# Kernel optimization log

Hardware: AMD Instinct MI355X
Metric: run time of the kernel (lower is better)

## Reference

```python
import jax, jax.numpy as jnp
import numpy as np

B, M, N, C, L = 4, 500, 500, 91, 3


def _lsa(cost):
    """Exact linear sum assignment (shortest augmenting path / LAPJV),
    numpy port of scipy's rectangular_lsap for a square cost matrix.
    Returns col4row: col4row[i] = column assigned to row i."""
    n = cost.shape[0]
    u = np.zeros(n, dtype=np.float64)
    v = np.zeros(n, dtype=np.float64)
    col4row = np.full(n, -1, dtype=np.int64)
    row4col = np.full(n, -1, dtype=np.int64)
    cost = cost.astype(np.float64)
    for cur_row in range(n):
        min_val = 0.0
        i = cur_row
        remaining = np.ones(n, dtype=bool)
        shortest = np.full(n, np.inf)
        path = np.full(n, -1, dtype=np.int64)
        SR = []
        sink = -1
        while sink == -1:
            SR.append(i)
            r = min_val + cost[i] - u[i] - v
            better = remaining & (r < shortest)
            shortest = np.where(better, r, shortest)
            path = np.where(better, i, path)
            masked = np.where(remaining, shortest, np.inf)
            j = int(np.argmin(masked))
            min_val = masked[j]
            remaining[j] = False
            if row4col[j] == -1:
                sink = j
            else:
                i = int(row4col[j])
        u[cur_row] += min_val
        sr = np.array(SR[1:], dtype=np.int64)
        if sr.size:
            u[sr] += min_val - shortest[col4row[sr]]
        scanned_cols = ~remaining
        v[scanned_cols] -= min_val - shortest[scanned_cols]
        # augment along the alternating path
        j = sink
        while True:
            i = int(path[j])
            row4col[j] = i
            col4row[i], j = j, col4row[i]
            if i == cur_row:
                break
    return col4row


def _assignment(cost_np):
    """(B, M, N) numpy cost -> (B, M) row->col mapping (square => all assigned)."""
    return np.stack([_lsa(c) for c in cost_np]).astype(np.int64)


def _cost_matrix(p2_boxes, p2_logits, p1_boxes, p1_logits):
    # center L2 distance: cdist(boxes2[..., :2], boxes1[..., :2], p=2) -> (B, M, N)
    diff = p2_boxes[:, :, None, :2] - p1_boxes[:, None, :, :2]
    center_d = jnp.sqrt(jnp.sum(diff * diff, axis=-1))
    # class disparity: cdist(sigmoid(l2), sigmoid(l1), p=inf) -> (B, M, N)
    s2 = jax.nn.sigmoid(p2_logits)
    s1 = jax.nn.sigmoid(p1_logits)
    class_d = jnp.max(jnp.abs(s2[:, :, None, :] - s1[:, None, :, :]), axis=-1)
    return 0.5 * center_d + 0.5 * class_d


def _extrapolate(p2_boxes, p2_logits, p1_boxes, p1_logits, mapping, factor):
    has = mapping != -1                      # (B, M)
    m = jnp.where(has, mapping, 0)
    idx4 = jnp.broadcast_to(m[:, :, None], m.shape + (4,))
    corr_b1 = jnp.take_along_axis(p1_boxes, idx4, axis=1)
    corr_b1 = jnp.where(has[:, :, None], corr_b1, p2_boxes)
    # 'linear' dim extrapolation, clamped at 0
    pos = p2_boxes[..., 0:2] + (p2_boxes[..., 0:2] - corr_b1[..., 0:2]) * factor
    dim = jnp.maximum(p2_boxes[..., 2:4] + (p2_boxes[..., 2:4] - corr_b1[..., 2:4]) * factor, 0.0)
    boxes3 = jnp.concatenate([pos, dim], axis=2)
    nclass = p1_logits.shape[-1]
    idxc = jnp.broadcast_to(m[:, :, None], m.shape + (nclass,))
    corr_l1 = jnp.take_along_axis(p1_logits, idxc, axis=1)
    corr_l1 = jnp.where(has[:, :, None], corr_l1, 0.0)
    logits3 = 0.5 * (p2_logits + corr_l1)
    return boxes3, logits3


def setup_inputs() -> dict:
    key = jax.random.key(0)
    k1, k2, k3, k4, k5 = jax.random.split(key, 5)
    pred1_boxes = jax.random.uniform(k1, (B, N, 4), dtype=jnp.float32)
    pred1_logits = jax.random.normal(k2, (B, N, C), dtype=jnp.float32)
    pred2_boxes = jax.random.uniform(k3, (B, M, 4), dtype=jnp.float32)
    pred2_logits = jax.random.normal(k4, (B, M, C), dtype=jnp.float32)
    # strictly increasing timestamps so offsets are positive
    temporal_offsets = jnp.cumsum(
        jax.random.uniform(k5, (B, L), minval=0.1, maxval=1.0, dtype=jnp.float32), axis=1)
    return {
        "pred1_boxes": pred1_boxes,
        "pred1_logits": pred1_logits,
        "pred2_boxes": pred2_boxes,
        "pred2_logits": pred2_logits,
        "temporal_offsets": temporal_offsets,
    }


def reference(pred1_boxes, pred1_logits, pred2_boxes, pred2_logits, temporal_offsets):
    cost = _cost_matrix(pred2_boxes, pred2_logits, pred1_boxes, pred1_logits)
    mapping = jnp.asarray(_assignment(np.asarray(cost)))  # (B, M) int64
    first = temporal_offsets[:, 1] - temporal_offsets[:, 0]
    second = temporal_offsets[:, 2] - temporal_offsets[:, 1]
    factor = (second / first)[:, None, None]
    boxes3, logits3 = _extrapolate(pred2_boxes, pred2_logits,
                                   pred1_boxes, pred1_logits, mapping, factor)
    return boxes3, logits3
```

## Files before the change

### kernel.cpp

```cpp
#include <hip/hip_runtime.h>
#include <math.h>

#define Bq 4
#define Mq 500
#define Nq 500
#define Cq 91
#define NPHASE 5

__device__ __forceinline__ float sigmoidf_(float x) {
    return 1.0f / (1.0f + expf(-x));
}

__global__ __launch_bounds__(256) void cost_kernel(
    const float* __restrict__ p1_boxes, const float* __restrict__ p1_logits,
    const float* __restrict__ p2_boxes, const float* __restrict__ p2_logits,
    float* __restrict__ cost)
{
    __shared__ float s2t[16][Cq + 1];
    __shared__ float s1t[16][Cq + 1];
    __shared__ float b2x[16], b2y[16], b1x[16], b1y[16];
    const int b  = blockIdx.z;
    const int i0 = blockIdx.y * 16;
    const int j0 = blockIdx.x * 16;
    const int tid = threadIdx.x;

    for (int t = tid; t < 16 * Cq; t += 256) {
        const int r = t / Cq, c = t - r * Cq;
        const int i = min(i0 + r, Mq - 1);
        const int j = min(j0 + r, Nq - 1);
        s2t[r][c] = sigmoidf_(p2_logits[((size_t)b * Mq + i) * Cq + c]);
        s1t[r][c] = sigmoidf_(p1_logits[((size_t)b * Nq + j) * Cq + c]);
    }
    if (tid < 16) {
        const int i = min(i0 + tid, Mq - 1);
        const int j = min(j0 + tid, Nq - 1);
        b2x[tid] = p2_boxes[((size_t)b * Mq + i) * 4 + 0];
        b2y[tid] = p2_boxes[((size_t)b * Mq + i) * 4 + 1];
        b1x[tid] = p1_boxes[((size_t)b * Nq + j) * 4 + 0];
        b1y[tid] = p1_boxes[((size_t)b * Nq + j) * 4 + 1];
    }
    __syncthreads();

    const int ty = tid >> 4, tx = tid & 15;
    const int i = i0 + ty, j = j0 + tx;
    if (i < Mq && j < Nq) {
        float mx = 0.0f;
        #pragma unroll 7
        for (int c = 0; c < Cq; ++c)
            mx = fmaxf(mx, fabsf(s2t[ty][c] - s1t[tx][c]));
        const float dx = b2x[ty] - b1x[tx];
        const float dy = b2y[ty] - b1y[tx];
        const float cd = sqrtf(dx * dx + dy * dy);
        cost[((size_t)b * Mq + i) * Nq + j] = 0.5f * cd + 0.5f * mx;
    }
}

__global__ __launch_bounds__(256) void colred_kernel(
    const float* __restrict__ cost, float* __restrict__ v0, int* __restrict__ amin)
{
    const int j = blockIdx.x * 256 + threadIdx.x;
    const int b = blockIdx.y;
    if (j >= Nq) return;
    const float* __restrict__ cb = cost + (size_t)b * Mq * Nq;
    float best = INFINITY;
    int bi = 0;
    #pragma unroll 4
    for (int i = 0; i < Mq; ++i) {
        const float c = cb[(size_t)i * Nq + j];
        if (c < best) { best = c; bi = i; }
    }
    v0[b * Nq + j] = best;
    amin[b * Nq + j] = bi;
}

template<int CTRL>
__device__ __forceinline__ float dppminv_(float x) {
    const int moved = __builtin_amdgcn_update_dpp(
        0x7F800000, __float_as_int(x), CTRL, 0xF, 0xF, false);
    return fminf(x, __int_as_float(moved));
}
__device__ __forceinline__ float wave_min_f32_(float x) {
    x = dppminv_<0x111>(x);
    x = dppminv_<0x112>(x);
    x = dppminv_<0x114>(x);
    x = dppminv_<0x118>(x);
    x = dppminv_<0x142>(x);
    x = dppminv_<0x143>(x);
    return __int_as_float(__builtin_amdgcn_readlane(__float_as_int(x), 63));
}

__device__ __forceinline__ void pairmin_(float& va, unsigned& pa, float vb, unsigned pb) {
    const bool le = (va <= vb);
    va = fminf(va, vb);
    pa = le ? pa : pb;
}

__device__ __forceinline__ unsigned long long pack_bid_(float p, int row) {
    return ((unsigned long long)__float_as_uint(p) << 32) | (unsigned)(row + 1);
}

__global__ __launch_bounds__(1024) void auction_kernel(
    const float* __restrict__ cost, const float* __restrict__ v0,
    const int* __restrict__ amin,
    float* __restrict__ v_out, int* __restrict__ owner_out)
{
    constexpr int n = Nq;
    __shared__ float p_lds[512];
    __shared__ int   owner_lds[512];
    __shared__ int   match_lds[512];
    __shared__ unsigned long long bid_lds[512];
    __shared__ int   flist[512];
    __shared__ int   jlist[512];
    __shared__ int   nfree_lds, njl_lds;

    const float eps_tab[NPHASE] = {4e-3f, 8e-4f, 1.6e-4f, 3.2e-5f, 0.0f};
    const int   cap_tab[NPHASE] = {48, 32, 32, 32, 64};

    const int tid = threadIdx.x;
    const int lane = tid & 63;
    const int wv = tid >> 6;
    const int b = blockIdx.x;
    const float* __restrict__ cb = cost + (size_t)b * n * n;

    const unsigned init_mask = (lane < 61) ? 0xFFu : 0x0Fu;
    const int off2 = (lane < 61) ? 256 + 4 * lane : 0;

    float v0_r[8];
    {
        const float4 a0 = *(const float4*)(v0 + b * n + 4 * lane);
        const float4 a1 = *(const float4*)(v0 + b * n + off2);
        const float vv[8] = {a0.x, a0.y, a0.z, a0.w, a1.x, a1.y, a1.z, a1.w};
        #pragma unroll
        for (int k = 0; k < 8; ++k)
            v0_r[k] = ((init_mask >> k) & 1) ? vv[k] : 0.0f;
    }
    if (tid < 512) {
        p_lds[tid] = 0.0f; owner_lds[tid] = -1; match_lds[tid] = -1;
        bid_lds[tid] = 0ull;
    }
    __syncthreads();
    if (tid < n) {
        const int i0 = amin[b * n + tid];
        if (atomicCAS(&match_lds[i0], -1, tid) == -1) owner_lds[tid] = i0;
    }
    __syncthreads();

    for (int ph = 0; ph < NPHASE; ++ph) {
        const float eps = eps_tab[ph];
        const int cap = cap_tab[ph];
        if (ph > 0) {
            if (tid < 512) { owner_lds[tid] = -1; match_lds[tid] = -1; }
        }
        __syncthreads();

        for (int round = 0; round < cap; ++round) {
            if (tid == 0) { nfree_lds = 0; njl_lds = 0; }
            __syncthreads();
            if (tid < n && match_lds[tid] < 0)
                flist[atomicAdd(&nfree_lds, 1)] = tid;
            __syncthreads();
            const int nf = nfree_lds;
            if (nf == 0) break;

            for (int idx = wv; idx < nf; idx += 16) {
                const int i = flist[idx];
                const float* __restrict__ crow = cb + (size_t)i * n;
                const float4 c0 = *(const float4*)(crow + 4 * lane);
                const float4 c1 = *(const float4*)(crow + off2);
                const float4 p0 = *(const float4*)&p_lds[4 * lane];
                const float4 p1 = *(const float4*)&p_lds[off2];
                const float cc[8] = {c0.x, c0.y, c0.z, c0.w, c1.x, c1.y, c1.z, c1.w};
                const float pp[8] = {p0.x, p0.y, p0.z, p0.w, p1.x, p1.y, p1.z, p1.w};
                float d[8]; unsigned pj[8];
                #pragma unroll
                for (int k = 0; k < 8; ++k) {
                    const int j = (k < 4) ? 4 * lane + k : 256 + 4 * lane + (k - 4);
                    d[k] = ((init_mask >> k) & 1) ? cc[k] - v0_r[k] + pp[k] : INFINITY;
                    pj[k] = (unsigned)j;
                }
                float    a0 = d[0], a1 = d[1], a2 = d[2], a3 = d[3];
                float    a4 = d[4], a5 = d[5], a6 = d[6], a7 = d[7];
                unsigned b0 = pj[0], b1 = pj[1], b2 = pj[2], b3 = pj[3];
                unsigned b4 = pj[4], b5 = pj[5], b6 = pj[6], b7 = pj[7];
                pairmin_(a0, b0, a1, b1);  pairmin_(a2, b2, a3, b3);
                pairmin_(a4, b4, a5, b5);  pairmin_(a6, b6, a7, b7);
                pairmin_(a0, b0, a2, b2);  pairmin_(a4, b4, a6, b6);
                pairmin_(a0, b0, a4, b4);
                const float lmin = a0;
                const unsigned lpay = b0;

                const float g1 = wave_min_f32_(lmin);
                const unsigned long long cm = __ballot(lmin == g1);
                const int wl = (int)__builtin_ctzll(cm);
                const int j1 = __builtin_amdgcn_readlane((int)lpay, wl);

                const int ow = (j1 >> 2) & 63, kw = ((j1 >> 8) << 2) | (j1 & 3);
                float lmin2 = INFINITY;
                #pragma unroll
                for (int k = 0; k < 8; ++k) {
                    const float dv = (k == kw && lane == ow) ? INFINITY : d[k];
                    lmin2 = fminf(lmin2, dv);
                }
                const float g2 = wave_min_f32_(lmin2);

                if (lane == 0) {
                    const float pnew = p_lds[j1] + (g2 - g1) + eps;
                    atomicMax(&bid_lds[j1], pack_bid_(pnew, i));
                    jlist[atomicAdd(&njl_lds, 1)] = j1;
                }
            }
            __syncthreads();

            const int nj = njl_lds;
            for (int t = tid; t < nj; t += 1024) {
                const int j = jlist[t];
                const unsigned long long bd = atomicExch(&bid_lds[j], 0ull);
                if (bd != 0ull) {
                    const int ri = (int)(bd & 0xFFFFFFFFull) - 1;
                    const float pn = __uint_as_float((unsigned)(bd >> 32));
                    const int prev = owner_lds[j];
                    if (prev >= 0) match_lds[prev] = -1;
                    owner_lds[j] = ri;
                    match_lds[ri] = j;
                    p_lds[j] = pn;
                }
            }
            __syncthreads();
        }
    }

    if (tid < n) {
        v_out[b * n + tid] = v0[b * n + tid] - p_lds[tid];
        owner_out[b * n + tid] = owner_lds[tid];
    }
}

__global__ __launch_bounds__(64) void lsa_kernel(
    const float* __restrict__ cost, const float* __restrict__ v_in,
    const int* __restrict__ owner_in, int* __restrict__ mapping)
{
    constexpr int n = Nq;
    __shared__ float u_lds[512];
    __shared__ float shortest_lds[512];
    __shared__ int   path_lds[512];
    __shared__ int   row4col_lds[512];
    __shared__ int   col4row_lds[512];

    const int lane = threadIdx.x;
    const int b = blockIdx.x;
    const float* __restrict__ cb = cost + (size_t)b * n * n;

    const unsigned init_mask = (lane < 61) ? 0xFFu : 0x0Fu;
    const int off2 = (lane < 61) ? 256 + 4 * lane : 0;

    float v_r[8], vwork_r[8], short_r[8], shortfin_r[8], t_r[8];
    int path_r[8];
    unsigned pay_r[8];

    {
        const float4 a0 = *(const float4*)(v_in + b * n + 4 * lane);
        const float4 a1 = *(const float4*)(v_in + b * n + off2);
        const float vv[8] = {a0.x, a0.y, a0.z, a0.w, a1.x, a1.y, a1.z, a1.w};
        #pragma unroll
        for (int k = 0; k < 8; ++k)
            v_r[k] = ((init_mask >> k) & 1) ? vv[k] : 0.0f;
    }
    for (int t = lane; t < 512; t += 64) {
        u_lds[t] = 0.0f; row4col_lds[t] = -1; col4row_lds[t] = -1;
    }
    __syncthreads();
    for (int t = lane; t < n; t += 64) {
        const int r = owner_in[b * n + t];
        if (r >= 0 && atomicCAS(&col4row_lds[r], -1, t) == -1)
            row4col_lds[t] = r;
    }
    __syncthreads();

    {
        int j1c = col4row_lds[0];
        float4 ta0 = *(const float4*)(cb + 4 * lane);
        float4 ta1 = *(const float4*)(cb + off2);
        for (int i2 = 0; i2 < n; ++i2) {
            const float4 c0 = ta0, c1 = ta1;
            const int j1 = j1c;
            const int inx = (i2 + 1 < n) ? i2 + 1 : i2;
            const float* __restrict__ crn = cb + (size_t)inx * n;
            ta0 = *(const float4*)(crn + 4 * lane);
            ta1 = *(const float4*)(crn + off2);
            j1c = col4row_lds[inx];
            if (j1 < 0) continue;
            const float cc[8] = {c0.x, c0.y, c0.z, c0.w, c1.x, c1.y, c1.z, c1.w};
            const int owner = (j1 >> 2) & 63;
            const int kwin  = ((j1 >> 8) << 2) | (j1 & 3);
            float d[8];
            float rcj = INFINITY;
            #pragma unroll
            for (int k = 0; k < 8; ++k) {
                const bool mine = (k == kwin && lane == owner);
                const bool use = ((init_mask >> k) & 1) && !mine;
                d[k] = use ? cc[k] - v_r[k] : INFINITY;
                if (mine) rcj = cc[k] - v_r[k];
            }
            const float mu = wave_min_f32_(
                fminf(fminf(fminf(d[0], d[1]), fminf(d[2], d[3])),
                      fminf(fminf(d[4], d[5]), fminf(d[6], d[7]))));
            const float rc1g = __int_as_float(
                __builtin_amdgcn_readlane(__float_as_int(rcj), owner));
            const bool keep = (rc1g <= mu);
            #pragma unroll
            for (int k = 0; k < 8; ++k)
                if (keep && k == kwin && lane == owner) v_r[k] = cc[k] - mu;
            if (lane == 0) {
                if (keep) u_lds[i2] = mu;
                else { row4col_lds[j1] = -1; col4row_lds[i2] = -1; }
            }
        }
    }
    __syncthreads();

    {
        const int4 r0 = *(const int4*)&row4col_lds[4 * lane];
        const int4 r1 = *(const int4*)&row4col_lds[off2];
        const int rr[8] = {r0.x, r0.y, r0.z, r0.w, r1.x, r1.y, r1.z, r1.w};
        #pragma unroll
        for (int k = 0; k < 8; ++k) {
            const int j = (k < 4) ? 4 * lane + k : 256 + 4 * lane + (k - 4);
            const bool valid = (init_mask >> k) & 1;
            pay_r[k] = valid ? (((unsigned)j << 10) | (unsigned)(rr[k] + 1))
                             : 0xFFFFFFFFu;
            vwork_r[k] = valid ? v_r[k] : -INFINITY;
            short_r[k] = INFINITY;
            shortfin_r[k] = INFINITY;
            path_r[k] = -1;
        }
    }
    for (int t = lane; t < n; t += 64)
        path_lds[t] = -1;
    unsigned sr_mask = 0;
    __syncthreads();

    for (int cur_row = 0; cur_row < n; ++cur_row) {
        if (col4row_lds[cur_row] >= 0) continue;

        int sink_j = -1;
        int i = cur_row;
        float min_val = 0.0f;
        const float* __restrict__ crow = cb + (size_t)i * n;
        float4 cv0 = *(const float4*)(crow + 4 * lane);
        float4 cv1 = *(const float4*)(crow + off2);
        float a = -u_lds[cur_row];

        for (int pops = 0; pops < n; ++pops) {
            if ((i & 63) == lane) sr_mask |= 1u << (i >> 6);

            #pragma unroll
            for (int k = 0; k < 8; ++k) t_r[k] = a - vwork_r[k];

            {
                const float c4[4] = {cv0.x, cv0.y, cv0.z, cv0.w};
                #pragma unroll
                for (int k = 0; k < 4; ++k) {
                    const float r = c4[k] + t_r[k];
                    if (r < short_r[k]) { short_r[k] = r; path_r[k] = i; }
                }
            }
            {
                const float c4[4] = {cv1.x, cv1.y, cv1.z, cv1.w};
                #pragma unroll
                for (int k = 0; k < 4; ++k) {
                    const float r = c4[k] + t_r[4 + k];
                    if (r < short_r[4 + k]) { short_r[4 + k] = r; path_r[4 + k] = i; }
                }
            }

            float    m0 = short_r[0], m1 = short_r[1], m2 = short_r[2], m3 = short_r[3];
            float    m4 = short_r[4], m5 = short_r[5], m6 = short_r[6], m7 = short_r[7];
            unsigned q0 = pay_r[0], q1 = pay_r[1], q2 = pay_r[2], q3 = pay_r[3];
            unsigned q4 = pay_r[4], q5 = pay_r[5], q6 = pay_r[6], q7 = pay_r[7];
            pairmin_(m0, q0, m1, q1);  pairmin_(m2, q2, m3, q3);
            pairmin_(m4, q4, m5, q5);  pairmin_(m6, q6, m7, q7);
            pairmin_(m0, q0, m2, q2);  pairmin_(m4, q4, m6, q6);
            pairmin_(m0, q0, m4, q4);
            const float lmin = m0;
            const unsigned lpay = q0;

            const float gmin = wave_min_f32_(lmin);
            const unsigned long long cand = __ballot(lmin == gmin);
            const int wl = (int)__builtin_ctzll(cand);
            const unsigned win = (unsigned)__builtin_amdgcn_readlane((int)lpay, wl);

            min_val = gmin;
            const unsigned jst = win >> 10;
            const unsigned rc1 = win & 0x3FFu;

            const int i_next = (int)rc1 - 1;
            const int i_safe = (i_next < 0) ? 0 : i_next;
            crow = cb + (size_t)i_safe * n;
            cv0 = *(const float4*)(crow + 4 * lane);
            cv1 = *(const float4*)(crow + off2);
            a = gmin - u_lds[i_safe];

            const int owner = (int)((jst >> 2) & 63u);
            const int kwin  = (int)(((jst >> 8) << 2) | (jst & 3u));
            #pragma unroll
            for (int k = 0; k < 8; ++k) {
                if (k == kwin && lane == owner) {
                    shortfin_r[k] = short_r[k];
                    short_r[k] = INFINITY;
                    vwork_r[k] = -INFINITY;
                }
            }

            if (rc1 == 0u) { sink_j = (int)jst; break; }
            i = i_next;
        }

        if (sink_j >= 0) {
            *(float4*)&shortest_lds[4 * lane] =
                make_float4(shortfin_r[0], shortfin_r[1], shortfin_r[2], shortfin_r[3]);
            *(int4*)&path_lds[4 * lane] =
                make_int4(path_r[0], path_r[1], path_r[2], path_r[3]);
            *(float4*)&shortest_lds[256 + 4 * lane] =
                make_float4(shortfin_r[4], shortfin_r[5], shortfin_r[6], shortfin_r[7]);
            *(int4*)&path_lds[256 + 4 * lane] =
                make_int4(path_r[4], path_r[5], path_r[6], path_r[7]);
            __syncthreads();

            #pragma unroll
            for (int k = 0; k < 8; ++k) {
                const int t = lane + (k << 6);
                if (t < n && (sr_mask & (1u << k))) {
                    if (t == cur_row) u_lds[t] += min_val;
                    else              u_lds[t] += min_val - shortest_lds[col4row_lds[t]];
                }
            }
            #pragma unroll
            for (int k = 0; k < 8; ++k) {
                if (((init_mask >> k) & 1) && vwork_r[k] == -INFINITY)
                    v_r[k] -= min_val - shortfin_r[k];
            }
            __syncthreads();

            if (lane == 0) {
                int j = sink_j;
                for (;;) {
                    const int ii = path_lds[j];
                    row4col_lds[j] = ii;
                    const int tmp = col4row_lds[ii];
                    col4row_lds[ii] = j;
                    j = tmp;
                    if (ii == cur_row) break;
                }
            }
            __syncthreads();
        }

        {
            const int4 r0 = *(const int4*)&row4col_lds[4 * lane];
            const int4 r1 = *(const int4*)&row4col_lds[off2];
            const int rr[8] = {r0.x, r0.y, r0.z, r0.w, r1.x, r1.y, r1.z, r1.w};
            #pragma unroll
            for (int k = 0; k < 8; ++k) {
                const int j = (k < 4) ? 4 * lane + k : 256 + 4 * lane + (k - 4);
                const bool valid = (init_mask >> k) & 1;
                pay_r[k] = valid ? (((unsigned)j << 10) | (unsigned)(rr[k] + 1))
                                 : 0xFFFFFFFFu;
                vwork_r[k] = valid ? v_r[k] : -INFINITY;
                short_r[k] = INFINITY;
                shortfin_r[k] = INFINITY;
                path_r[k] = -1;
            }
        }
        sr_mask = 0;
        __syncthreads();
    }

    for (int t = lane; t < n; t += 64)
        mapping[b * n + t] = col4row_lds[t];
}

__global__ __launch_bounds__(256) void extrap_boxes_kernel(
    const float* __restrict__ p1_boxes, const float* __restrict__ p2_boxes,
    const float* __restrict__ toffs, const int* __restrict__ mapping,
    float* __restrict__ out_boxes)
{
    const int idx = blockIdx.x * blockDim.x + threadIdx.x;
    if (idx >= Bq * Mq) return;
    const int b = idx / Mq;
    const float t0 = toffs[b * 3 + 0], t1 = toffs[b * 3 + 1], t2 = toffs[b * 3 + 2];
    const float factor = (t2 - t1) / (t1 - t0);
    const int m = mapping[idx];
    const float4 p2 = ((const float4*)p2_boxes)[idx];
    const float4 p1 = (m >= 0) ? ((const float4*)p1_boxes)[b * Nq + m] : p2;
    float4 o;
    o.x = p2.x + (p2.x - p1.x) * factor;
    o.y = p2.y + (p2.y - p1.y) * factor;
    o.z = fmaxf(p2.z + (p2.z - p1.z) * factor, 0.0f);
    o.w = fmaxf(p2.w + (p2.w - p1.w) * factor, 0.0f);
    ((float4*)out_boxes)[idx] = o;
}

__global__ __launch_bounds__(256) void extrap_logits_kernel(
    const float* __restrict__ p1_logits, const float* __restrict__ p2_logits,
    const int* __restrict__ mapping, float* __restrict__ out_logits)
{
    const int idx = blockIdx.x * blockDim.x + threadIdx.x;
    if (idx >= Bq * Mq * Cq) return;
    const int c = idx % Cq;
    const int bi = idx / Cq;
    const int b = bi / Mq;
    const int m = mapping[bi];
    const float corr = (m >= 0) ? p1_logits[((size_t)b * Nq + m) * Cq + c] : 0.0f;
    out_logits[idx] = 0.5f * (p2_logits[idx] + corr);
}

extern "C" void kernel_launch(void* const* d_in, const int* in_sizes, int n_in,
                              void* d_out, int out_size, void* d_ws, size_t ws_size,
                              hipStream_t stream) {
    const float* p1_boxes  = (const float*)d_in[0];
    const float* p1_logits = (const float*)d_in[1];
    const float* p2_boxes  = (const float*)d_in[2];
    const float* p2_logits = (const float*)d_in[3];
    const float* toffs     = (const float*)d_in[4];
    float* out = (float*)d_out;

    char* ws = (char*)d_ws;
    float* cost    = (float*)ws;
    int*   mapping = (int*)  (ws + 4000000);
    float* v0      = (float*)(ws + 4008000);
    int*   amin    = (int*)  (ws + 4016000);
    float* v_auc   = (float*)(ws + 4024000);
    int*   owner   = (int*)  (ws + 4032000);

    dim3 cgrid((Nq + 15) / 16, (Mq + 15) / 16, Bq);
    cost_kernel<<<cgrid, 256, 0, stream>>>(p1_boxes, p1_logits, p2_boxes, p2_logits, cost);

    colred_kernel<<<dim3(2, Bq), 256, 0, stream>>>(cost, v0, amin);

    auction_kernel<<<Bq, 1024, 0, stream>>>(cost, v0, amin, v_auc, owner);

    lsa_kernel<<<Bq, 64, 0, stream>>>(cost, v_auc, owner, mapping);

    extrap_boxes_kernel<<<(Bq * Mq + 255) / 256, 256, 0, stream>>>(
        p1_boxes, p2_boxes, toffs, mapping, out);
    extrap_logits_kernel<<<(Bq * Mq * Cq + 255) / 256, 256, 0, stream>>>(
        p1_logits, p2_logits, mapping, out + Bq * Mq * 4);
}
```

Measured before the change: 2.045 ms.

## Use multi-source shortest augmenting paths seeded from all free rows in LSA

Each augmentation now runs its Dijkstra search from every still-unassigned row at once, instead of from one row at a time. All free rows' cost rows are relaxed up front with a prefetched row stream, and the free-row list is kept in LDS and compacted after each augmentation. The dual updates and path reconstruction are adjusted to suit: all sources get min_val added, and augmentation stops at the first unmatched row. The aim is to shorten the serial chain of pop-and-reduce steps, each of which is latency-bound. The cost is a scan of all free rows at the start of every augmentation, which grows quadratically with the number of free rows.

```diff
diff --git a/kernel.cpp b/kernel.cpp
--- a/kernel.cpp
+++ b/kernel.cpp
@@ -245,6 +245,8 @@
     __shared__ int   path_lds[512];
     __shared__ int   row4col_lds[512];
     __shared__ int   col4row_lds[512];
+    __shared__ int   fr_lds[512];
+    __shared__ int   nfr_lds;
 
     const int lane = threadIdx.x;
     const int b = blockIdx.x;
@@ -318,142 +320,15 @@
     }
     __syncthreads();
 
-    {
-        const int4 r0 = *(const int4*)&row4col_lds[4 * lane];
-        const int4 r1 = *(const int4*)&row4col_lds[off2];
-        const int rr[8] = {r0.x, r0.y, r0.z, r0.w, r1.x, r1.y, r1.z, r1.w};
-        #pragma unroll
-        for (int k = 0; k < 8; ++k) {
-            const int j = (k < 4) ? 4 * lane + k : 256 + 4 * lane + (k - 4);
-            const bool valid = (init_mask >> k) & 1;
-            pay_r[k] = valid ? (((unsigned)j << 10) | (unsigned)(rr[k] + 1))
-                             : 0xFFFFFFFFu;
-            vwork_r[k] = valid ? v_r[k] : -INFINITY;
-            short_r[k] = INFINITY;
-            shortfin_r[k] = INFINITY;
-            path_r[k] = -1;
-        }
-    }
+    if (lane == 0) nfr_lds = 0;
+    __syncthreads();
     for (int t = lane; t < n; t += 64)
-        path_lds[t] = -1;
-    unsigned sr_mask = 0;
-    __syncthreads();
-
-    for (int cur_row = 0; cur_row < n; ++cur_row) {
-        if (col4row_lds[cur_row] >= 0) continue;
-
-        int sink_j = -1;
-        int i = cur_row;
-        float min_val = 0.0f;
-        const float* __restrict__ crow = cb + (size_t)i * n;
-        float4 cv0 = *(const float4*)(crow + 4 * lane);
-        float4 cv1 = *(const float4*)(crow + off2);
-        float a = -u_lds[cur_row];
-
-        for (int pops = 0; pops < n; ++pops) {
-            if ((i & 63) == lane) sr_mask |= 1u << (i >> 6);
-
-            #pragma unroll
-            for (int k = 0; k < 8; ++k) t_r[k] = a - vwork_r[k];
-
-            {
-                const float c4[4] = {cv0.x, cv0.y, cv0.z, cv0.w};
-                #pragma unroll
-                for (int k = 0; k < 4; ++k) {
-                    const float r = c4[k] + t_r[k];
-                    if (r < short_r[k]) { short_r[k] = r; path_r[k] = i; }
-                }
-            }
-            {
-                const float c4[4] = {cv1.x, cv1.y, cv1.z, cv1.w};
-                #pragma unroll
-                for (int k = 0; k < 4; ++k) {
-                    const float r = c4[k] + t_r[4 + k];
-                    if (r < short_r[4 + k]) { short_r[4 + k] = r; path_r[4 + k] = i; }
-                }
-            }
-
-            float    m0 = short_r[0], m1 = short_r[1], m2 = short_r[2], m3 = short_r[3];
-            float    m4 = short_r[4], m5 = short_r[5], m6 = short_r[6], m7 = short_r[7];
-            unsigned q0 = pay_r[0], q1 = pay_r[1], q2 = pay_r[2], q3 = pay_r[3];
-            unsigned q4 = pay_r[4], q5 = pay_r[5], q6 = pay_r[6], q7 = pay_r[7];
-            pairmin_(m0, q0, m1, q1);  pairmin_(m2, q2, m3, q3);
-            pairmin_(m4, q4, m5, q5);  pairmin_(m6, q6, m7, q7);
-            pairmin_(m0, q0, m2, q2);  pairmin_(m4, q4, m6, q6);
-            pairmin_(m0, q0, m4, q4);
-            const float lmin = m0;
-            const unsigned lpay = q0;
-
-            const float gmin = wave_min_f32_(lmin);
-            const unsigned long long cand = __ballot(lmin == gmin);
-            const int wl = (int)__builtin_ctzll(cand);
-            const unsigned win = (unsigned)__builtin_amdgcn_readlane((int)lpay, wl);
-
-            min_val = gmin;
-            const unsigned jst = win >> 10;
-            const unsigned rc1 = win & 0x3FFu;
-
-            const int i_next = (int)rc1 - 1;
-            const int i_safe = (i_next < 0) ? 0 : i_next;
-            crow = cb + (size_t)i_safe * n;
-            cv0 = *(const float4*)(crow + 4 * lane);
-            cv1 = *(const float4*)(crow + off2);
-            a = gmin - u_lds[i_safe];
-
-            const int owner = (int)((jst >> 2) & 63u);
-            const int kwin  = (int)(((jst >> 8) << 2) | (jst & 3u));
-            #pragma unroll
-            for (int k = 0; k < 8; ++k) {
-                if (k == kwin && lane == owner) {
-                    shortfin_r[k] = short_r[k];
-                    short_r[k] = INFINITY;
-                    vwork_r[k] = -INFINITY;
-                }
-            }
-
-            if (rc1 == 0u) { sink_j = (int)jst; break; }
-            i = i_next;
-        }
-
-        if (sink_j >= 0) {
-            *(float4*)&shortest_lds[4 * lane] =
-                make_float4(shortfin_r[0], shortfin_r[1], shortfin_r[2], shortfin_r[3]);
-            *(int4*)&path_lds[4 * lane] =
-                make_int4(path_r[0], path_r[1], path_r[2], path_r[3]);
-            *(float4*)&shortest_lds[256 + 4 * lane] =
-                make_float4(shortfin_r[4], shortfin_r[5], shortfin_r[6], shortfin_r[7]);
-            *(int4*)&path_lds[256 + 4 * lane] =
-                make_int4(path_r[4], path_r[5], path_r[6], path_r[7]);
-            __syncthreads();
-
-            #pragma unroll
-            for (int k = 0; k < 8; ++k) {
-                const int t = lane + (k << 6);
-                if (t < n && (sr_mask & (1u << k))) {
-                    if (t == cur_row) u_lds[t] += min_val;
-                    else              u_lds[t] += min_val - shortest_lds[col4row_lds[t]];
-                }
-            }
-            #pragma unroll
-            for (int k = 0; k < 8; ++k) {
-                if (((init_mask >> k) & 1) && vwork_r[k] == -INFINITY)
-                    v_r[k] -= min_val - shortfin_r[k];
-            }
-            __syncthreads();
-
-            if (lane == 0) {
-                int j = sink_j;
-                for (;;) {
-                    const int ii = path_lds[j];
-                    row4col_lds[j] = ii;
-                    const int tmp = col4row_lds[ii];
-                    col4row_lds[ii] = j;
-                    j = tmp;
-                    if (ii == cur_row) break;
-                }
-            }
-            __syncthreads();
-        }
+        if (col4row_lds[t] < 0) fr_lds[atomicAdd(&nfr_lds, 1)] = t;
+    __syncthreads();
+
+    for (int aug = 0; aug < n; ++aug) {
+        const int nfr = nfr_lds;
+        if (nfr == 0) break;
 
         {
             const int4 r0 = *(const int4*)&row4col_lds[4 * lane];
@@ -471,7 +346,154 @@
                 path_r[k] = -1;
             }
         }
-        sr_mask = 0;
+
+        {
+            int fi = fr_lds[0];
+            const float* __restrict__ crow = cb + (size_t)fi * n;
+            float4 s0 = *(const float4*)(crow + 4 * lane);
+            float4 s1 = *(const float4*)(crow + off2);
+            for (int t = 0; t < nfr; ++t) {
+                const float4 c0 = s0, c1 = s1;
+                const int cur_fi = fi;
+                const int tn = (t + 1 < nfr) ? t + 1 : t;
+                fi = fr_lds[tn];
+                const float* __restrict__ crn = cb + (size_t)fi * n;
+                s0 = *(const float4*)(crn + 4 * lane);
+                s1 = *(const float4*)(crn + off2);
+                const float a = -u_lds[cur_fi];
+                #pragma unroll
+                for (int k = 0; k < 8; ++k) t_r[k] = a - vwork_r[k];
+                const float cvk[8] = {c0.x, c0.y, c0.z, c0.w,
+                                      c1.x, c1.y, c1.z, c1.w};
+                #pragma unroll
+                for (int k = 0; k < 8; ++k) {
+                    const float r = cvk[k] + t_r[k];
+                    if (r < short_r[k]) { short_r[k] = r; path_r[k] = cur_fi; }
+                }
+            }
+        }
+
+        int sink_j = -1;
+        float min_val = 0.0f;
+        unsigned sr_mask = 0;
+        bool have_cv = false;
+        float4 cv0, cv1;
+        float a = 0.0f;
+        int i_cur = -1;
+
+        for (int pops = 0; pops <= n; ++pops) {
+            if (have_cv) {
+                #pragma unroll
+                for (int k = 0; k < 8; ++k) t_r[k] = a - vwork_r[k];
+                {
+                    const float c4[4] = {cv0.x, cv0.y, cv0.z, cv0.w};
+                    #pragma unroll
+                    for (int k = 0; k < 4; ++k) {
+                        const float r = c4[k] + t_r[k];
+                        if (r < short_r[k]) { short_r[k] = r; path_r[k] = i_cur; }
+                    }
+                }
+                {
+                    const float c4[4] = {cv1.x, cv1.y, cv1.z, cv1.w};
+                    #pragma unroll
+                    for (int k = 0; k < 4; ++k) {
+                        const float r = c4[k] + t_r[4 + k];
+                        if (r < short_r[4 + k]) { short_r[4 + k] = r; path_r[4 + k] = i_cur; }
+                    }
+                }
+            }
+
+            float    m0 = short_r[0], m1 = short_r[1], m2 = short_r[2], m3 = short_r[3];
+            float    m4 = short_r[4], m5 = short_r[5], m6 = short_r[6], m7 = short_r[7];
+            unsigned q0 = pay_r[0], q1 = pay_r[1], q2 = pay_r[2], q3 = pay_r[3];
+            unsigned q4 = pay_r[4], q5 = pay_r[5], q6 = pay_r[6], q7 = pay_r[7];
+            pairmin_(m0, q0, m1, q1);  pairmin_(m2, q2, m3, q3);
+            pairmin_(m4, q4, m5, q5);  pairmin_(m6, q6, m7, q7);
+            pairmin_(m0, q0, m2, q2);  pairmin_(m4, q4, m6, q6);
+            pairmin_(m0, q0, m4, q4);
+            const float lmin = m0;
+            const unsigned lpay = q0;
+
+            const float gmin = wave_min_f32_(lmin);
+            const unsigned long long cand = __ballot(lmin == gmin);
+            const int wl = (int)__builtin_ctzll(cand);
+            const unsigned win = (unsigned)__builtin_amdgcn_readlane((int)lpay, wl);
+
+            min_val = gmin;
+            const unsigned jst = win >> 10;
+            const unsigned rc1 = win & 0x3FFu;
+
+            const int i_next = (int)rc1 - 1;
+            const int i_safe = (i_next < 0) ? 0 : i_next;
+            const float* __restrict__ crow2 = cb + (size_t)i_safe * n;
+            cv0 = *(const float4*)(crow2 + 4 * lane);
+            cv1 = *(const float4*)(crow2 + off2);
+            a = gmin - u_lds[i_safe];
+
+            const int owner = (int)((jst >> 2) & 63u);
+            const int kwin  = (int)(((jst >> 8) << 2) | (jst & 3u));
+            #pragma unroll
+            for (int k = 0; k < 8; ++k) {
+                if (k == kwin && lane == owner) {
+                    shortfin_r[k] = short_r[k];
+                    short_r[k] = INFINITY;
+                    vwork_r[k] = -INFINITY;
+                }
+            }
+
+            if (rc1 == 0u) { sink_j = (int)jst; break; }
+            if ((i_next & 63) == lane) sr_mask |= 1u << (i_next >> 6);
+            i_cur = i_next;
+            have_cv = true;
+        }
+
+        if (sink_j < 0) break;
+
+        *(float4*)&shortest_lds[4 * lane] =
+            make_float4(shortfin_r[0], shortfin_r[1], shortfin_r[2], shortfin_r[3]);
+        *(int4*)&path_lds[4 * lane] =
+            make_int4(path_r[0], path_r[1], path_r[2], path_r[3]);
+        *(float4*)&shortest_lds[256 + 4 * lane] =
+            make_float4(shortfin_r[4], shortfin_r[5], shortfin_r[6], shortfin_r[7]);
+        *(int4*)&path_lds[256 + 4 * lane] =
+            make_int4(path_r[4], path_r[5], path_r[6], path_r[7]);
+        __syncthreads();
+
+        #pragma unroll
+        for (int k = 0; k < 8; ++k) {
+            const int t = lane + (k << 6);
+            if (t < n && (sr_mask & (1u << k)))
+                u_lds[t] += min_val - shortest_lds[col4row_lds[t]];
+        }
+        for (int t = lane; t < nfr; t += 64)
+            u_lds[fr_lds[t]] += min_val;
+        #pragma unroll
+        for (int k = 0; k < 8; ++k) {
+            if (((init_mask >> k) & 1) && vwork_r[k] == -INFINITY)
+                v_r[k] -= min_val - shortfin_r[k];
+        }
+        __syncthreads();
+
+        if (lane == 0) {
+            int j = sink_j;
+            int origin = -1;
+            for (;;) {
+                const int ii = path_lds[j];
+                row4col_lds[j] = ii;
+                const int tmp = col4row_lds[ii];
+                col4row_lds[ii] = j;
+                if (tmp < 0) { origin = ii; break; }
+                j = tmp;
+            }
+            const int m = nfr_lds;
+            for (int t = 0; t < m; ++t) {
+                if (fr_lds[t] == origin) {
+                    fr_lds[t] = fr_lds[m - 1];
+                    break;
+                }
+            }
+            nfr_lds = m - 1;
+        }
         __syncthreads();
     }
 
```

Result: no change. 2.005 ms (-1.9%).
